# Kernel optimization log

Measured on AMD Instinct MI355X. Metric: run time of the kernel, lower is better.

Reference implementation:

```python
import jax, jax.numpy as jnp
import numpy as np

# ViT-Tiny + Performer attention (eval mode: dropout/droppath are no-ops)
B = 64
IMG, PATCH, GRID = 224, 16, 14
NPATCH, NTOK = 196, 197
EMBED, HEADS, HEAD_DIM = 192, 3, 64
DEPTH, FEAT, MLP, NCLS = 12, 256, 768, 1000
EXIT_IDXS = [4, 8, 12]
LN_EPS = 1e-5


def _ln(x, w, b):
    mu = x.mean(-1, keepdims=True)
    var = ((x - mu) ** 2).mean(-1, keepdims=True)
    return (x - mu) / jnp.sqrt(var + LN_EPS) * w + b


def setup_inputs() -> dict:
    key = jax.random.key(0)
    ks = jax.random.split(key, 16)
    n = lambda k, shape, s=0.02: jax.random.normal(k, shape, jnp.float32) * s
    inp = {}
    inp["x"] = jax.random.normal(ks[0], (B, 3, IMG, IMG), jnp.float32)
    inp["patch_w"] = n(ks[1], (EMBED, 3, PATCH, PATCH))
    inp["patch_b"] = jnp.zeros((EMBED,), jnp.float32)
    inp["pe_norm_w"] = jnp.ones((EMBED,), jnp.float32)
    inp["pe_norm_b"] = jnp.zeros((EMBED,), jnp.float32)
    inp["cls_token"] = n(ks[2], (1, 1, EMBED))
    inp["pos_embed"] = n(ks[3], (1, NTOK, EMBED))
    inp["norm1_w"] = jnp.ones((DEPTH, EMBED), jnp.float32)
    inp["norm1_b"] = jnp.zeros((DEPTH, EMBED), jnp.float32)
    inp["qkv_w"] = n(ks[4], (DEPTH, EMBED, 3 * EMBED))
    inp["qkv_b"] = jnp.zeros((DEPTH, 3 * EMBED), jnp.float32)
    # Gaussian random projection matrix (stands in for the orthogonal RF matrix)
    inp["proj_mat"] = jax.random.normal(ks[5], (DEPTH, FEAT, HEAD_DIM), jnp.float32)
    inp["attn_proj_w"] = n(ks[6], (DEPTH, EMBED, EMBED))
    inp["attn_proj_b"] = jnp.zeros((DEPTH, EMBED), jnp.float32)
    inp["norm2_w"] = jnp.ones((DEPTH, EMBED), jnp.float32)
    inp["norm2_b"] = jnp.zeros((DEPTH, EMBED), jnp.float32)
    inp["fc1_w"] = n(ks[7], (DEPTH, EMBED, MLP))
    inp["fc1_b"] = jnp.zeros((DEPTH, MLP), jnp.float32)
    inp["fc2_w"] = n(ks[8], (DEPTH, MLP, EMBED))
    inp["fc2_b"] = jnp.zeros((DEPTH, EMBED), jnp.float32)
    inp["exit_w"] = n(ks[9], (len(EXIT_IDXS), EMBED, NCLS))
    inp["exit_b"] = jnp.zeros((len(EXIT_IDXS), NCLS), jnp.float32)
    inp["final_norm_w"] = jnp.ones((EMBED,), jnp.float32)
    inp["final_norm_b"] = jnp.zeros((EMBED,), jnp.float32)
    inp["head_w"] = n(ks[10], (EMBED, NCLS))
    inp["head_b"] = jnp.zeros((NCLS,), jnp.float32)
    return inp


def _performer_attn(x, qw, qb, pm, pw, pb):
    Bn, N, C = x.shape
    qkv = (x @ qw + qb).reshape(Bn, N, 3, HEADS, HEAD_DIM).transpose(2, 0, 3, 1, 4)
    q, k, v = qkv[0], qkv[1], qkv[2]  # [B,H,N,d]

    def fmap(t):
        proj = jnp.einsum('bhnd,fd->bhnf', t, pm)  # random-feature projection
        norm_t = jnp.sum(t * t, axis=-1, keepdims=True) / 2.0
        return jnp.exp(proj - norm_t) * (HEAD_DIM ** -0.25)

    pq = fmap(q)  # [B,H,N,F]
    pk = fmap(k)
    k_cumsum = pk.sum(axis=2)  # [B,H,F]
    D_inv = 1.0 / jnp.einsum('bhnf,bhf->bhn', pq, k_cumsum)
    attn = jnp.einsum('bhnf,bhmf->bhnm', pq, pk)  # as in original (materializes NxN)
    out = jnp.einsum('bhnm,bhmd->bhnd', attn, v)
    out = out * D_inv[..., None]
    out = out.transpose(0, 2, 1, 3).reshape(Bn, N, C)
    return out @ pw + pb


def reference(x, patch_w, patch_b, pe_norm_w, pe_norm_b, cls_token, pos_embed,
              norm1_w, norm1_b, qkv_w, qkv_b, proj_mat, attn_proj_w, attn_proj_b,
              norm2_w, norm2_b, fc1_w, fc1_b, fc2_w, fc2_b,
              exit_w, exit_b, final_norm_w, final_norm_b, head_w, head_b):
    Bn = x.shape[0]
    # PatchEmbed: non-overlapping 16x16 conv == reshape + matmul (c,ph,pw order)
    p = x.reshape(Bn, 3, GRID, PATCH, GRID, PATCH).transpose(0, 2, 4, 1, 3, 5)
    p = p.reshape(Bn, NPATCH, 3 * PATCH * PATCH)
    tok = p @ patch_w.reshape(EMBED, -1).T + patch_b
    tok = _ln(tok, pe_norm_w, pe_norm_b)
    cls = jnp.broadcast_to(cls_token, (Bn, 1, EMBED))
    h = jnp.concatenate([cls, tok], axis=1) + pos_embed  # [B,197,192]

    exits = []
    for i in range(DEPTH):
        a = _performer_attn(_ln(h, norm1_w[i], norm1_b[i]), qkv_w[i], qkv_b[i],
                            proj_mat[i], attn_proj_w[i], attn_proj_b[i])
        h = h + a
        m = _ln(h, norm2_w[i], norm2_b[i])
        m = jax.nn.gelu(m @ fc1_w[i] + fc1_b[i], approximate=False) @ fc2_w[i] + fc2_b[i]
        h = h + m
        if (i + 1) in EXIT_IDXS:
            e = EXIT_IDXS.index(i + 1)
            z = h.mean(axis=1)  # AdaptiveAvgPool1d(1) over tokens
            exits.append(z @ exit_w[e] + exit_b[e])

    hf = _ln(h, final_norm_w, final_norm_b)
    logits = hf[:, 0] @ head_w + head_b  # cls-token head
    return (logits, exits[0], exits[1], exits[2])
```

## Files before the change

### kernel.cpp

```cpp
#include <hip/hip_runtime.h>
#include <math.h>

typedef unsigned short u16;
typedef unsigned int u32;
typedef __attribute__((ext_vector_type(8))) short short8;
typedef __attribute__((ext_vector_type(4))) float floatx4;

#define BB 64
#define NTOK 197
#define NPATCH 196
#define EMB 192
#define NH 3
#define HD 64
#define FEAT 256
#define MLPD 768
#define NCLS 1000
#define MTOT (BB*NTOK)
#define MPAT (BB*NPATCH)
#define BHT (BB*NH)

__device__ __forceinline__ u16 f2bf(float x) {
    u32 u = __builtin_bit_cast(u32, x);
    u32 r = u + 0x7FFFu + ((u >> 16) & 1u);
    return (u16)(r >> 16);
}
__device__ __forceinline__ float bf2f(u16 u) {
    return __builtin_bit_cast(float, (u32)u << 16);
}
__device__ __forceinline__ float sqr8bf(uint4 v) {
    float s = 0.f;
    float t;
    t = bf2f((u16)(v.x & 0xffff)); s += t*t;  t = bf2f((u16)(v.x >> 16)); s += t*t;
    t = bf2f((u16)(v.y & 0xffff)); s += t*t;  t = bf2f((u16)(v.y >> 16)); s += t*t;
    t = bf2f((u16)(v.z & 0xffff)); s += t*t;  t = bf2f((u16)(v.z >> 16)); s += t*t;
    t = bf2f((u16)(v.w & 0xffff)); s += t*t;  t = bf2f((u16)(v.w >> 16)); s += t*t;
    return s;
}

__global__ void cvt_bf16(const float* __restrict__ in, u16* __restrict__ out, int n)
{
    const int i = blockIdx.x * 256 + threadIdx.x;
    if (i < n) out[i] = f2bf(in[i]);
}

__global__ void tr_bf16_t(const float* __restrict__ in, u16* __restrict__ out,
                          int R, int C)
{
    __shared__ u16 t[32][33];
    const int l = blockIdx.z;
    const int c0 = blockIdx.x * 32, r0 = blockIdx.y * 32;
    const int tx = threadIdx.x & 31, ty = threadIdx.x >> 5;
    const float* ip = in + ((size_t)l * R + r0) * C + c0;
#pragma unroll
    for (int j = 0; j < 4; ++j)
        t[ty + j*8][tx] = f2bf(ip[(size_t)(ty + j*8) * C + tx]);
    __syncthreads();
    u16* op = out + ((size_t)l * C + c0) * R + r0;
#pragma unroll
    for (int j = 0; j < 4; ++j)
        op[(size_t)(ty + j*8) * R + tx] = t[tx][ty + j*8];
}

__global__ __launch_bounds__(256) void gemm_bf16(
    const u16* __restrict__ A, const u16* __restrict__ Bt,
    const float* __restrict__ bias,
    float* __restrict__ Cf, u16* __restrict__ Cb,
    int M, int N, int K, int mode, int ntx)
{
    __shared__ u16 As[128][72];
    __shared__ u16 Bs[64][72];
    const int tid = threadIdx.x;
    const int lane = tid & 63, wave = tid >> 6;
    const int l16 = lane & 15, quad = lane >> 4;
    const int nwg = gridDim.x;
    const int q = nwg >> 3, r = nwg & 7;
    const int xcd = blockIdx.x & 7, jj = blockIdx.x >> 3;
    const int wg = (xcd < r ? xcd * (q + 1) : r * (q + 1) + (xcd - r) * q) + jj;
// ... 73 lines not shown
        for (int cf = 0; cf < 4; ++cf) {
            const int lc = cf * 16 + l16;
            const float bia = bias[n0 + lc];
#pragma unroll
            for (int reg = 0; reg < 4; ++reg) {
                const int lr = wave * 32 + rf * 16 + quad * 4 + reg;
                float v = acc[rf][cf][reg] + bia;
                if (mode == 2)
                    v = 0.5f * v * (1.f + erff(v * 0.70710678118654752f));
                const int phys = (((lc >> 3) ^ (lr & 7)) << 3) | (lc & 7);
                As[lr][phys] = f2bf(v);
            }
        }
    }
    __syncthreads();
#pragma unroll
    for (int it = 0; it < 4; ++it) {
        const int idx = it * 256 + tid;
        const int row = idx >> 3, c8 = idx & 7;
        const int pc8 = c8 ^ (row & 7);
        const uint4 val = *(const uint4*)&As[row][pc8 * 8];
        const int gm = m0 + row;
        if (gm < M)
            *(uint4*)&Cb[(size_t)gm * N + n0 + c8 * 8] = val;
    }
}

__global__ __launch_bounds__(256) void gemm_ln(
    const u16* __restrict__ A, const u16* __restrict__ Bt,
    const float* __restrict__ bias,
    const float* __restrict__ lnw, const float* __restrict__ lnb,
    float* __restrict__ H, u16* __restrict__ outb, int K)
{
    __shared__ u16 As[64][72];
    __shared__ u16 Bs[192][72];
    __shared__ float red_s[2][64][2];
    const int tid = threadIdx.x;
    const int lane = tid & 63, wave = tid >> 6;
    const int wr = wave & 1, wc = wave >> 1;
    const int l16 = lane & 15, quad = lane >> 4;
    const int m0 = blockIdx.x * 64;
    const int srow = tid >> 2, skof = (tid & 3) * 16;

    floatx4 acc[2][6];
#pragma unroll
    for (int i = 0; i < 2; ++i)
#pragma unroll
        for (int j = 0; j < 6; ++j) acc[i][j] = (floatx4){0.f,0.f,0.f,0.f};

    const u16* ap = A + (size_t)(m0 + srow) * K + skof;
    const u16* bp = Bt + (size_t)srow * K + skof;
    const size_t bstep = (size_t)64 * K;

    for (int k0 = 0; k0 < K; k0 += 64) {
        const uint4 a0 = *(const uint4*)(ap + k0);
        const uint4 a1 = *(const uint4*)(ap + k0 + 8);
        const uint4 b0 = *(const uint4*)(bp + k0);
        const uint4 b1 = *(const uint4*)(bp + k0 + 8);
        const uint4 b2 = *(const uint4*)(bp + bstep + k0);
        const uint4 b3 = *(const uint4*)(bp + bstep + k0 + 8);
        const uint4 b4 = *(const uint4*)(bp + 2*bstep + k0);
        const uint4 b5 = *(const uint4*)(bp + 2*bstep + k0 + 8);
        if (k0) __syncthreads();
        *(uint4*)&As[srow][skof]           = a0;
        *(uint4*)&As[srow][skof + 8]       = a1;
        *(uint4*)&Bs[srow][skof]           = b0;
        *(uint4*)&Bs[srow][skof + 8]       = b1;
        *(uint4*)&Bs[srow + 64][skof]      = b2;
        *(uint4*)&Bs[srow + 64][skof + 8]  = b3;
        *(uint4*)&Bs[srow + 128][skof]     = b4;
        *(uint4*)&Bs[srow + 128][skof + 8] = b5;
        __syncthreads();
#pragma unroll
        for (int ks = 0; ks < 2; ++ks) {
            short8 af[2], bf[6];
#pragma unroll
            for (int rf = 0; rf < 2; ++rf)
                af[rf] = *(const short8*)&As[wr*32 + rf*16 + l16][ks*32 + quad*8];
#pragma unroll
            for (int cf = 0; cf < 6; ++cf)
                bf[cf] = *(const short8*)&Bs[wc*96 + cf*16 + l16][ks*32 + quad*8];
#pragma unroll
            for (int rf = 0; rf < 2; ++rf)
#pragma unroll
                for (int cf = 0; cf < 6; ++cf)
                    acc[rf][cf] = __builtin_amdgcn_mfma_f32_16x16x32_bf16(af[rf], bf[cf], acc[rf][cf], 0, 0, 0);
        }
    }

    float s_[2][4], q_[2][4];
#pragma unroll
    for (int rf = 0; rf < 2; ++rf)
#pragma unroll
        for (int reg = 0; reg < 4; ++reg) { s_[rf][reg] = 0.f; q_[rf][reg] = 0.f; }

#pragma unroll
    for (int rf = 0; rf < 2; ++rf) {
#pragma unroll
        for (int cf = 0; cf < 6; ++cf) {
            const int gn = wc * 96 + cf * 16 + l16;
            const float bia = bias[gn];
#pragma unroll
            for (int reg = 0; reg < 4; ++reg) {
                const int gm = m0 + wr * 32 + rf * 16 + quad * 4 + reg;
                float v = acc[rf][cf][reg] + bia + H[(size_t)gm * EMB + gn];
                H[(size_t)gm * EMB + gn] = v;
                acc[rf][cf][reg] = v;
                s_[rf][reg] += v;
                q_[rf][reg] += v * v;
            }
        }
    }

    if (lnw) {
#pragma unroll
        for (int rf = 0; rf < 2; ++rf)
#pragma unroll
            for (int reg = 0; reg < 4; ++reg) {
                float s = s_[rf][reg], q = q_[rf][reg];
                s += __shfl_xor(s, 1); q += __shfl_xor(q, 1);
                s += __shfl_xor(s, 2); q += __shfl_xor(q, 2);
                s += __shfl_xor(s, 4); q += __shfl_xor(q, 4);
                s += __shfl_xor(s, 8); q += __shfl_xor(q, 8);
                if (l16 == 0) {
                    const int rl = wr * 32 + rf * 16 + quad * 4 + reg;
                    red_s[wc][rl][0] = s;
                    red_s[wc][rl][1] = q;
                }
            }
        __syncthreads();
#pragma unroll
        for (int rf = 0; rf < 2; ++rf) {
#pragma unroll
            for (int reg = 0; reg < 4; ++reg) {
                const int rl = wr * 32 + rf * 16 + quad * 4 + reg;
                const float ts = red_s[0][rl][0] + red_s[1][rl][0];
                const float tq = red_s[0][rl][1] + red_s[1][rl][1];
                const float mu = ts * (1.f / 192.f);
                const float var = tq * (1.f / 192.f) - mu * mu;
                const float rstd = rsqrtf(fmaxf(var, 0.f) + 1e-5f);
                const int gm = m0 + rl;
#pragma unroll
                for (int cf = 0; cf < 6; ++cf) {
                    const int gn = wc * 96 + cf * 16 + l16;
                    const float y = (acc[rf][cf][reg] - mu) * rstd * lnw[gn] + lnb[gn];
                    outb[(size_t)gm * EMB + gn] = f2bf(y);
                }
            }
        }
    }
}

__global__ __launch_bounds__(256) void attn_pkv(
    const u16* __restrict__ qkv, const u16* __restrict__ pmb,
    u16* __restrict__ kvT, float* __restrict__ ksum)
{
    __shared__ u16 pm_s[256][72];
    __shared__ u16 kt_s[64][72];
    __shared__ u16 vT_s[64][72];
    __shared__ u16 pkT_s[256][72];
    __shared__ float nrm_s[64];
    __shared__ float ksum_s[256];

    const int tid = threadIdx.x;
    const int lane = tid & 63, wave = tid >> 6;
    const int l16 = lane & 15, quad = lane >> 4;
    const int bh = blockIdx.x, b = bh / NH, h = bh % NH;
    const int fbase = wave * 64;
    const int srow = tid >> 2, skof = (tid & 3) * 16;
    const float scale = 0.35355339059327373f;

#pragma unroll
    for (int j = 0; j < 8; ++j) {
        const int flat = j * 256 + tid;
        const int f = flat >> 3, o = (flat & 7) * 8;
        *(uint4*)&pm_s[f][o] = *(const uint4*)(pmb + f * 64 + o);
    }
    ksum_s[tid] = 0.f;

    floatx4 kv[4][4];
#pragma unroll
    for (int i = 0; i < 4; ++i)
#pragma unroll
        for (int j = 0; j < 4; ++j) kv[i][j] = (floatx4){0.f,0.f,0.f,0.f};

    uint4 k0v = {0,0,0,0}, k1v = {0,0,0,0}, v0v = {0,0,0,0}, v1v = {0,0,0,0};
    {
        const u16* kp = qkv + ((size_t)(b * NTOK + srow)) * 576 + 192 + h * 64 + skof;
        k0v = *(const uint4*)kp; k1v = *(const uint4*)(kp + 8);
        v0v = *(const uint4*)(kp + 192); v1v = *(const uint4*)(kp + 200);
    }

    for (int t = 0; t < 4; ++t) {
        const int ncur = t * 64 + srow;
        if (t) __syncthreads();
        *(uint4*)&kt_s[srow][skof]     = k0v;
        *(uint4*)&kt_s[srow][skof + 8] = k1v;
        {
            u16 vv[16];
            vv[0]=(u16)(v0v.x&0xffff);  vv[1]=(u16)(v0v.x>>16);
            vv[2]=(u16)(v0v.y&0xffff);  vv[3]=(u16)(v0v.y>>16);
            vv[4]=(u16)(v0v.z&0xffff);  vv[5]=(u16)(v0v.z>>16);
            vv[6]=(u16)(v0v.w&0xffff);  vv[7]=(u16)(v0v.w>>16);
            vv[8]=(u16)(v1v.x&0xffff);  vv[9]=(u16)(v1v.x>>16);
            vv[10]=(u16)(v1v.y&0xffff); vv[11]=(u16)(v1v.y>>16);
            vv[12]=(u16)(v1v.z&0xffff); vv[13]=(u16)(v1v.z>>16);
            vv[14]=(u16)(v1v.w&0xffff); vv[15]=(u16)(v1v.w>>16);
#pragma unroll
            for (int j = 0; j < 16; ++j) vT_s[skof + j][srow] = vv[j];
        }
        float sq = sqr8bf(k0v) + sqr8bf(k1v);
        sq += __shfl_xor(sq, 1);
        sq += __shfl_xor(sq, 2);
        if ((tid & 3) == 0) nrm_s[srow] = (ncur < NTOK) ? 0.5f * sq : 1e30f;
        __syncthreads();

        if (t < 3) {
            const int n = (t + 1) * 64 + srow;
            k0v = (uint4){0,0,0,0}; k1v = (uint4){0,0,0,0};
            v0v = (uint4){0,0,0,0}; v1v = (uint4){0,0,0,0};
            if (n < NTOK) {
                const u16* kp = qkv + ((size_t)(b * NTOK + n)) * 576 + 192 + h * 64 + skof;
                k0v = *(const uint4*)kp; k1v = *(const uint4*)(kp + 8);
                v0v = *(const uint4*)(kp + 192); v1v = *(const uint4*)(kp + 200);
            }
        }

        floatx4 pa[4][4];
#pragma unroll
        for (int i = 0; i < 4; ++i)
#pragma unroll
            for (int j = 0; j < 4; ++j) pa[i][j] = (floatx4){0.f,0.f,0.f,0.f};
#pragma unroll
        for (int ks = 0; ks < 2; ++ks) {
            short8 a[4], bb[4];
#pragma unroll
            for (int rf = 0; rf < 4; ++rf)
                a[rf] = *(const short8*)&kt_s[rf*16 + l16][ks*32 + quad*8];
#pragma unroll
            for (int cf = 0; cf < 4; ++cf)
                bb[cf] = *(const short8*)&pm_s[fbase + cf*16 + l16][ks*32 + quad*8];
#pragma unroll
            for (int rf = 0; rf < 4; ++rf)
#pragma unroll
                for (int cf = 0; cf < 4; ++cf)
                    pa[rf][cf] = __builtin_amdgcn_mfma_f32_16x16x32_bf16(a[rf], bb[cf], pa[rf][cf], 0, 0, 0);
        }

        float ksp[4] = {0.f, 0.f, 0.f, 0.f};
#pragma unroll
        for (int rf = 0; rf < 4; ++rf) {
            const int nl = rf * 16 + quad * 4;
            const float nr0 = nrm_s[nl + 0], nr1 = nrm_s[nl + 1];
            const float nr2 = nrm_s[nl + 2], nr3 = nrm_s[nl + 3];
#pragma unroll
            for (int cf = 0; cf < 4; ++cf) {
                const int f = fbase + cf * 16 + l16;
                const u16 b0 = f2bf(__expf(pa[rf][cf][0] - nr0) * scale);
                const u16 b1 = f2bf(__expf(pa[rf][cf][1] - nr1) * scale);
                const u16 b2 = f2bf(__expf(pa[rf][cf][2] - nr2) * scale);
                const u16 b3 = f2bf(__expf(pa[rf][cf][3] - nr3) * scale);
                ksp[cf] += bf2f(b0) + bf2f(b1) + bf2f(b2) + bf2f(b3);
                *(u32*)&pkT_s[f][nl]     = (u32)b0 | ((u32)b1 << 16);
                *(u32*)&pkT_s[f][nl + 2] = (u32)b2 | ((u32)b3 << 16);
            }
        }
#pragma unroll
        for (int cf = 0; cf < 4; ++cf) {
            float v = ksp[cf];
            v += __shfl_xor(v, 16);
            v += __shfl_xor(v, 32);
            if (quad == 0) ksum_s[fbase + cf*16 + l16] += v;
        }

#pragma unroll
        for (int ks = 0; ks < 2; ++ks) {
            short8 a[4], bb[4];
#pragma unroll
            for (int rf = 0; rf < 4; ++rf)
                a[rf] = *(const short8*)&vT_s[rf*16 + l16][ks*32 + quad*8];
#pragma unroll
            for (int cf = 0; cf < 4; ++cf)
                bb[cf] = *(const short8*)&pkT_s[fbase + cf*16 + l16][ks*32 + quad*8];
#pragma unroll
            for (int rf = 0; rf < 4; ++rf)
#pragma unroll
                for (int cf = 0; cf < 4; ++cf)
                    kv[rf][cf] = __builtin_amdgcn_mfma_f32_16x16x32_bf16(a[rf], bb[cf], kv[rf][cf], 0, 0, 0);
        }
    }

    __syncthreads();
    ksum[(size_t)bh * 256 + tid] = ksum_s[tid];
#pragma unroll
    for (int rf = 0; rf < 4; ++rf)
#pragma unroll
        for (int cf = 0; cf < 4; ++cf) {
            const int f = fbase + cf * 16 + l16;
#pragma unroll
            for (int reg = 0; reg < 4; ++reg) {
                const int d = rf * 16 + quad * 4 + reg;
                kvT[((size_t)bh * 64 + d) * 256 + f] = f2bf(kv[rf][cf][reg]);
            }
        }
}

__global__ __launch_bounds__(256) void attn_out(
    const u16* __restrict__ qkv, const u16* __restrict__ pmb,
    const u16* __restrict__ kvT, const float* __restrict__ ksum,
    u16* __restrict__ attn_o)
{
    __shared__ u16 pm_s[256][72];
    __shared__ u16 q_s[64][72];
    __shared__ u16 pq_s[64][264];
    __shared__ u16 kv_s[64][264];
    __shared__ float nrm_s[64];
    __shared__ float den_s[4][64];

    const int tid = threadIdx.x;
    const int lane = tid & 63, wave = tid >> 6;
    const int l16 = lane & 15, quad = lane >> 4;
    const int bh = blockIdx.y, b = bh / NH, h = bh % NH;
    const int n0 = blockIdx.x * 64;
    const int fbase = wave * 64;
    const int srow = tid >> 2, skof = (tid & 3) * 16;
    const float scale = 0.35355339059327373f;

#pragma unroll
    for (int j = 0; j < 8; ++j) {
        const int flat = j * 256 + tid;
        const int f = flat >> 3, o = (flat & 7) * 8;
        *(uint4*)&pm_s[f][o] = *(const uint4*)(pmb + f * 64 + o);
    }
#pragma unroll
    for (int j = 0; j < 8; ++j) {
        const int flat = j * 256 + tid;
        const int d = flat >> 5, o = (flat & 31) * 8;
// ... 103 lines not shown
                oc[rf][cf] = __builtin_amdgcn_mfma_f32_16x16x32_bf16(a[rf], bb[cf], oc[rf][cf], 0, 0, 0);
    }

#pragma unroll
    for (int rf = 0; rf < 2; ++rf) {
#pragma unroll
        for (int reg = 0; reg < 4; ++reg) {
            const int nl = wr*32 + rf*16 + quad*4 + reg;
            const int gn = n0 + nl;
            if (gn >= NTOK) continue;
            const float di = 1.f / (den_s[0][nl] + den_s[1][nl] + den_s[2][nl] + den_s[3][nl]);
#pragma unroll
            for (int cf = 0; cf < 2; ++cf) {
                const int d = wc*32 + cf*16 + l16;
                attn_o[((size_t)(b * NTOK + gn)) * EMB + h * 64 + d] =
                    f2bf(oc[rf][cf][reg] * di);
            }
        }
    }
}

__global__ void im2col_kernel(const float* __restrict__ x, u16* __restrict__ p, int total)
{
    const int i = blockIdx.x * 256 + threadIdx.x;
    if (i >= total) return;
    const int col = i % 768, row = i / 768;
    const int px = col & 15, py = (col >> 4) & 15, c = col >> 8;
    const int gx = row % 14, gy = (row / 14) % 14, b = row / 196;
    p[i] = f2bf(x[((size_t)(b * 3 + c) * 224 + gy * 16 + py) * 224 + gx * 16 + px]);
}

__global__ void embed_finish(const float* __restrict__ tok, const float* __restrict__ cls,
                             const float* __restrict__ pos, const float* __restrict__ w,
                             const float* __restrict__ b, float* __restrict__ h)
{
    const int wid = threadIdx.x >> 6, lane = threadIdx.x & 63;
    const int r = blockIdx.x * 4 + wid;
    if (r >= MTOT) return;
    const int bb = r / NTOK, t = r % NTOK;
    float* q = h + (size_t)r * EMB;
    if (t == 0) {
        q[lane]       = cls[lane]       + pos[lane];
        q[lane + 64]  = cls[lane + 64]  + pos[lane + 64];
        q[lane + 128] = cls[lane + 128] + pos[lane + 128];
        return;
    }
    const float* p = tok + ((size_t)bb * NPATCH + (t - 1)) * EMB;
    float x0 = p[lane], x1 = p[lane + 64], x2 = p[lane + 128];
    float s = x0 + x1 + x2;
#pragma unroll
    for (int off = 32; off; off >>= 1) s += __shfl_xor(s, off);
    const float mu = s * (1.f / 192.f);
    const float d0 = x0 - mu, d1 = x1 - mu, d2 = x2 - mu;
    float v = d0 * d0 + d1 * d1 + d2 * d2;
#pragma unroll
    for (int off = 32; off; off >>= 1) v += __shfl_xor(v, off);
    const float rstd = rsqrtf(v * (1.f / 192.f) + 1e-5f);
    const float* pr = pos + (size_t)t * EMB;
    q[lane]       = d0 * rstd * w[lane]       + b[lane]       + pr[lane];
    q[lane + 64]  = d1 * rstd * w[lane + 64]  + b[lane + 64]  + pr[lane + 64];
    q[lane + 128] = d2 * rstd * w[lane + 128] + b[lane + 128] + pr[lane + 128];
}

__global__ void ln192(const float* __restrict__ in, int in_stride,
                      const float* __restrict__ w, const float* __restrict__ b,
                      u16* __restrict__ outb, float* __restrict__ outf, int rows)
{
    const int wid = threadIdx.x >> 6, lane = threadIdx.x & 63;
    const int r = blockIdx.x * 4 + wid;
    if (r >= rows) return;
    const float* p = in + (size_t)r * in_stride;
    float x0 = p[lane], x1 = p[lane + 64], x2 = p[lane + 128];
    float s = x0 + x1 + x2;
#pragma unroll
    for (int off = 32; off; off >>= 1) s += __shfl_xor(s, off);
    const float mu = s * (1.f / 192.f);
    const float d0 = x0 - mu, d1 = x1 - mu, d2 = x2 - mu;
    float v = d0 * d0 + d1 * d1 + d2 * d2;
#pragma unroll
    for (int off = 32; off; off >>= 1) v += __shfl_xor(v, off);
    const float rstd = rsqrtf(v * (1.f / 192.f) + 1e-5f);
    const float y0 = d0 * rstd * w[lane]       + b[lane];
    const float y1 = d1 * rstd * w[lane + 64]  + b[lane + 64];
    const float y2 = d2 * rstd * w[lane + 128] + b[lane + 128];
    if (outf) {
        float* q = outf + (size_t)r * EMB;
        q[lane] = y0; q[lane + 64] = y1; q[lane + 128] = y2;
    } else {
        u16* q = outb + (size_t)r * EMB;
        q[lane] = f2bf(y0); q[lane + 64] = f2bf(y1); q[lane + 128] = f2bf(y2);
    }
}

__global__ __launch_bounds__(256) void gemm_f32(
    const float* __restrict__ A, const float* __restrict__ Bm,
    const float* __restrict__ bias, float* __restrict__ C,
    int M, int N, int K)
{
    __shared__ float As[16][68];
    __shared__ float Bs[16][64];
    const int tid = threadIdx.x;
    const int tx = tid & 15, ty = tid >> 4;
    const int m0 = blockIdx.y * 64, n0 = blockIdx.x * 64;
    float acc[4][4] = {};

    for (int k0 = 0; k0 < K; k0 += 16) {
        {
            const int c = tid & 15, r4 = tid >> 4;
#pragma unroll
            for (int i = 0; i < 4; ++i) {
                const int r = r4 + i * 16, gm = m0 + r;
                As[c][r] = (gm < M) ? A[(size_t)gm * K + (k0 + c)] : 0.f;
            }
        }
        {
            const int cb = tid & 63, rb4 = tid >> 6;
#pragma unroll
            for (int i = 0; i < 4; ++i) {
                const int rb = rb4 + i * 4;
                const int gn = n0 + cb;
                Bs[rb][cb] = (gn < N) ? Bm[(size_t)(k0 + rb) * N + gn] : 0.f;
            }
        }
        __syncthreads();
#pragma unroll
        for (int kk = 0; kk < 16; ++kk) {
            const float4 av = *reinterpret_cast<const float4*>(&As[kk][ty * 4]);
            const float4 bv = *reinterpret_cast<const float4*>(&Bs[kk][tx * 4]);
            const float a_[4] = {av.x, av.y, av.z, av.w};
            const float b_[4] = {bv.x, bv.y, bv.z, bv.w};
#pragma unroll
            for (int i2 = 0; i2 < 4; ++i2)
#pragma unroll
                for (int j2 = 0; j2 < 4; ++j2)
                    acc[i2][j2] = fmaf(a_[i2], b_[j2], acc[i2][j2]);
        }
        __syncthreads();
    }

#pragma unroll
    for (int i = 0; i < 4; ++i) {
        const int gm = m0 + ty * 4 + i;
        if (gm >= M) continue;
#pragma unroll
        for (int j = 0; j < 4; ++j) {
            const int gn = n0 + tx * 4 + j;
            if (gn >= N) continue;
            C[(size_t)gm * N + gn] = acc[i][j] + bias[gn];
        }
    }
}

__global__ void pool_kernel(const float* __restrict__ h, float* __restrict__ pooled)
{
    __shared__ float red[192];
    const int b = blockIdx.x;
    const int slice = threadIdx.x / 192;
    const int e = threadIdx.x % 192;
    float s = 0.f;
    for (int n = slice; n < NTOK; n += 2)
        s += h[((size_t)(b * NTOK + n)) * EMB + e];
    if (slice == 1) red[e] = s;
    __syncthreads();
    if (slice == 0)
        pooled[b * EMB + e] = (s + red[e]) * (1.f / 197.f);
}

extern "C" void kernel_launch(void* const* d_in, const int* in_sizes, int n_in,
                              void* d_out, int out_size, void* d_ws, size_t ws_size,
                              hipStream_t stream)
{
    const float* x          = (const float*)d_in[0];
    const float* patch_w    = (const float*)d_in[1];
    const float* patch_b    = (const float*)d_in[2];
    const float* pe_norm_w  = (const float*)d_in[3];
    const float* pe_norm_b  = (const float*)d_in[4];
    const float* cls_token  = (const float*)d_in[5];
    const float* pos_embed  = (const float*)d_in[6];
    const float* norm1_w    = (const float*)d_in[7];
    const float* norm1_b    = (const float*)d_in[8];
    const float* qkv_w      = (const float*)d_in[9];
    const float* qkv_b      = (const float*)d_in[10];
    const float* proj_mat   = (const float*)d_in[11];
    const float* attn_pw    = (const float*)d_in[12];
    const float* attn_pb    = (const float*)d_in[13];
    const float* norm2_w    = (const float*)d_in[14];
    const float* norm2_b    = (const float*)d_in[15];
    const float* fc1_w      = (const float*)d_in[16];
    const float* fc1_b      = (const float*)d_in[17];
    const float* fc2_w      = (const float*)d_in[18];
    const float* fc2_b      = (const float*)d_in[19];
    const float* exit_w     = (const float*)d_in[20];
    const float* exit_b     = (const float*)d_in[21];
    const float* fnorm_w    = (const float*)d_in[22];
    const float* fnorm_b    = (const float*)d_in[23];
    const float* head_w     = (const float*)d_in[24];
    const float* head_b     = (const float*)d_in[25];
    float* out = (float*)d_out;

    float* ws = (float*)d_ws;
    float* H     = ws + 0;
    u16*   QKVB  = (u16*)(ws + 2420736);
    u16*   XLNB  = (u16*)(ws + 6051840);
    u16*   KVT   = (u16*)(ws + 19968000);
    u16*   MIDB  = (u16*)(ws + 21540864);
    u16*   ATNB  = (u16*)(ws + 26382336);
    float* XLNF  = ws + 27592704;
    float* POOL  = ws + 27604992;
    float* KSUM  = ws + 27617280;
    u16*   QKVWT = (u16*)(ws + 27666432);
    u16*   APWT  = (u16*)(ws + 28329984);
    u16*   F1WT  = (u16*)(ws + 28551168);
    u16*   F2WT  = (u16*)(ws + 29435904);
    u16*   PATWB = (u16*)(ws + 30320640);
    u16*   PMB   = (u16*)(ws + 30394368);
    u16*   P_IMB = MIDB;
    float* TOK   = (float*)QKVB;

    if (ws_size < (size_t)30492672 * sizeof(float)) return;

    cvt_bf16<<<(147456 + 255) / 256, 256, 0, stream>>>(patch_w, PATWB, 147456);
    cvt_bf16<<<(196608 + 255) / 256, 256, 0, stream>>>(proj_mat, PMB, 196608);
    tr_bf16_t<<<dim3(18, 6, 12), 256, 0, stream>>>(qkv_w,   QKVWT, 192, 576);
    tr_bf16_t<<<dim3(6, 6, 12),  256, 0, stream>>>(attn_pw, APWT,  192, 192);
    tr_bf16_t<<<dim3(24, 6, 12), 256, 0, stream>>>(fc1_w,   F1WT,  192, 768);
    tr_bf16_t<<<dim3(6, 24, 12), 256, 0, stream>>>(fc2_w,   F2WT,  768, 192);

    im2col_kernel<<<(MPAT * 768 + 255) / 256, 256, 0, stream>>>(x, P_IMB, MPAT * 768);
    gemm_bf16<<<294, 256, 0, stream>>>(P_IMB, PATWB, patch_b,
                                       TOK, nullptr, MPAT, EMB, 768, 0, 3);
    embed_finish<<<(MTOT + 3) / 4, 256, 0, stream>>>(TOK, cls_token, pos_embed,
                                                     pe_norm_w, pe_norm_b, H);
    ln192<<<(MTOT + 3) / 4, 256, 0, stream>>>(H, EMB, norm1_w, norm1_b,
                                              XLNB, nullptr, MTOT);

    for (int i = 0; i < 12; ++i) {
        const u16* qwt  = QKVWT + (size_t)i * 576 * 192;
        const u16* pwt  = APWT  + (size_t)i * 192 * 192;
        const u16* f1wt = F1WT  + (size_t)i * 768 * 192;
        const u16* f2wt = F2WT  + (size_t)i * 192 * 768;
        const u16* pmb  = PMB   + (size_t)i * 256 * 64;
        const float* qb  = qkv_b   + (size_t)i * 576;
        const float* pb  = attn_pb + (size_t)i * 192;
        const float* f1b = fc1_b   + (size_t)i * 768;
        const float* f2b = fc2_b   + (size_t)i * 192;

        gemm_bf16<<<891, 256, 0, stream>>>(XLNB, qwt, qb,
                                           nullptr, QKVB, MTOT, 576, 192, 3, 9);
        attn_pkv<<<dim3(BHT), 256, 0, stream>>>(QKVB, pmb, KVT, KSUM);
        attn_out<<<dim3(4, BHT), 256, 0, stream>>>(QKVB, pmb, KVT, KSUM, ATNB);
        gemm_ln<<<197, 256, 0, stream>>>(ATNB, pwt, pb,
                                         norm2_w + (size_t)i * EMB, norm2_b + (size_t)i * EMB,
                                         H, XLNB, EMB);
        gemm_bf16<<<1188, 256, 0, stream>>>(XLNB, f1wt, f1b,
                                            nullptr, MIDB, MTOT, MLPD, 192, 2, 12);
        const float* nw = (i < 11) ? norm1_w + (size_t)(i + 1) * EMB : nullptr;
        const float* nb = (i < 11) ? norm1_b + (size_t)(i + 1) * EMB : nullptr;
        gemm_ln<<<197, 256, 0, stream>>>(MIDB, f2wt, f2b, nw, nb, H, XLNB, MLPD);

        const int e = (i == 3) ? 0 : (i == 7) ? 1 : (i == 11) ? 2 : -1;
        if (e >= 0) {
            pool_kernel<<<BB, 384, 0, stream>>>(H, POOL);
            gemm_f32<<<dim3(16, 1), 256, 0, stream>>>(POOL, exit_w + (size_t)e * 192 * 1000,
                                                      exit_b + (size_t)e * 1000,
                                                      out + (size_t)(1 + e) * BB * NCLS,
                                                      BB, NCLS, EMB);
        }
    }

    ln192<<<(BB + 3) / 4, 256, 0, stream>>>(H, NTOK * EMB, fnorm_w, fnorm_b,
                                            nullptr, XLNF, BB);
    gemm_f32<<<dim3(16, 1), 256, 0, stream>>>(XLNF, head_w, head_b, out, BB, NCLS, EMB);
}
```

Before: 1.540 ms.

## Split attention and LN-GEMM across more blocks, fuse embed LN, MFMA classifier heads

Several changes land together. gemm_ln tiles are cut from 64 to 32 rows, doubling the grid to 394 blocks, and attn_pkv is split across four feature-quarter blocks per batch-head, both to raise occupancy on a GPU with many CUs. The first norm1 LayerNorm is folded into embed_finish, which removes one launch and one pass over H. The fp32 exit and head GEMMs become bf16 MFMA kernels on pre-transposed weights, at some cost in precision for the classifier outputs.

Measured after the change: 1.391 ms. 1.11x faster.

```diff
diff --git a/kernel.cpp b/kernel.cpp
--- a/kernel.cpp
+++ b/kernel.cpp
@@ -43,6 +43,17 @@
     if (i < n) out[i] = f2bf(in[i]);
 }
 
+__global__ void tr_bf16(const float* __restrict__ in, u16* __restrict__ out,
+                        int R, int C, int total)
+{
+    const int i = blockIdx.x * 256 + threadIdx.x;
+    if (i >= total) return;
+    const int r = i % R;
+    const int c = (i / R) % C;
+    const int l = i / (R * C);
+    out[i] = f2bf(in[((size_t)l * R + r) * C + c]);
+}
+
 __global__ void tr_bf16_t(const float* __restrict__ in, u16* __restrict__ out,
                           int R, int C)
 {
@@ -182,29 +193,28 @@
     const float* __restrict__ lnw, const float* __restrict__ lnb,
     float* __restrict__ H, u16* __restrict__ outb, int K)
 {
-    __shared__ u16 As[64][72];
+    __shared__ u16 As[32][72];
     __shared__ u16 Bs[192][72];
-    __shared__ float red_s[2][64][2];
+    __shared__ float red_s[2][32][2];
     const int tid = threadIdx.x;
     const int lane = tid & 63, wave = tid >> 6;
-    const int wr = wave & 1, wc = wave >> 1;
+    const int wr = wave & 1;
+    const int wc = wave >> 1;
     const int l16 = lane & 15, quad = lane >> 4;
-    const int m0 = blockIdx.x * 64;
+    const int m0 = blockIdx.x * 32;
+    const int srowA = tid >> 3, skofA = (tid & 7) * 8;
     const int srow = tid >> 2, skof = (tid & 3) * 16;
 
-    floatx4 acc[2][6];
-#pragma unroll
-    for (int i = 0; i < 2; ++i)
-#pragma unroll
-        for (int j = 0; j < 6; ++j) acc[i][j] = (floatx4){0.f,0.f,0.f,0.f};
-
-    const u16* ap = A + (size_t)(m0 + srow) * K + skof;
+    floatx4 acc[6];
+#pragma unroll
+    for (int j = 0; j < 6; ++j) acc[j] = (floatx4){0.f,0.f,0.f,0.f};
+
+    const u16* ap = A + (size_t)(m0 + srowA) * K + skofA;
     const u16* bp = Bt + (size_t)srow * K + skof;
     const size_t bstep = (size_t)64 * K;
 
     for (int k0 = 0; k0 < K; k0 += 64) {
         const uint4 a0 = *(const uint4*)(ap + k0);
-        const uint4 a1 = *(const uint4*)(ap + k0 + 8);
         const uint4 b0 = *(const uint4*)(bp + k0);
         const uint4 b1 = *(const uint4*)(bp + k0 + 8);
         const uint4 b2 = *(const uint4*)(bp + bstep + k0);
@@ -212,8 +222,7 @@
         const uint4 b4 = *(const uint4*)(bp + 2*bstep + k0);
         const uint4 b5 = *(const uint4*)(bp + 2*bstep + k0 + 8);
         if (k0) __syncthreads();
-        *(uint4*)&As[srow][skof]           = a0;
-        *(uint4*)&As[srow][skof + 8]       = a1;
+        *(uint4*)&As[srowA][skofA]         = a0;
         *(uint4*)&Bs[srow][skof]           = b0;
         *(uint4*)&Bs[srow][skof + 8]       = b1;
         *(uint4*)&Bs[srow + 64][skof]      = b2;
@@ -223,79 +232,65 @@
         __syncthreads();
 #pragma unroll
         for (int ks = 0; ks < 2; ++ks) {
-            short8 af[2], bf[6];
-#pragma unroll
-            for (int rf = 0; rf < 2; ++rf)
-                af[rf] = *(const short8*)&As[wr*32 + rf*16 + l16][ks*32 + quad*8];
+            const short8 af = *(const short8*)&As[wr*16 + l16][ks*32 + quad*8];
+            short8 bf[6];
 #pragma unroll
             for (int cf = 0; cf < 6; ++cf)
                 bf[cf] = *(const short8*)&Bs[wc*96 + cf*16 + l16][ks*32 + quad*8];
 #pragma unroll
-            for (int rf = 0; rf < 2; ++rf)
-#pragma unroll
-                for (int cf = 0; cf < 6; ++cf)
-                    acc[rf][cf] = __builtin_amdgcn_mfma_f32_16x16x32_bf16(af[rf], bf[cf], acc[rf][cf], 0, 0, 0);
-        }
-    }
-
-    float s_[2][4], q_[2][4];
-#pragma unroll
-    for (int rf = 0; rf < 2; ++rf)
-#pragma unroll
-        for (int reg = 0; reg < 4; ++reg) { s_[rf][reg] = 0.f; q_[rf][reg] = 0.f; }
-
-#pragma unroll
-    for (int rf = 0; rf < 2; ++rf) {
-#pragma unroll
-        for (int cf = 0; cf < 6; ++cf) {
-            const int gn = wc * 96 + cf * 16 + l16;
-            const float bia = bias[gn];
-#pragma unroll
-            for (int reg = 0; reg < 4; ++reg) {
-                const int gm = m0 + wr * 32 + rf * 16 + quad * 4 + reg;
-                float v = acc[rf][cf][reg] + bia + H[(size_t)gm * EMB + gn];
-                H[(size_t)gm * EMB + gn] = v;
-                acc[rf][cf][reg] = v;
-                s_[rf][reg] += v;
-                q_[rf][reg] += v * v;
+            for (int cf = 0; cf < 6; ++cf)
+                acc[cf] = __builtin_amdgcn_mfma_f32_16x16x32_bf16(af, bf[cf], acc[cf], 0, 0, 0);
+        }
+    }
+
+    float s_[4], q_[4];
+#pragma unroll
+    for (int reg = 0; reg < 4; ++reg) { s_[reg] = 0.f; q_[reg] = 0.f; }
+
+#pragma unroll
+    for (int cf = 0; cf < 6; ++cf) {
+        const int gn = wc * 96 + cf * 16 + l16;
+        const float bia = bias[gn];
+#pragma unroll
+        for (int reg = 0; reg < 4; ++reg) {
+            const int gm = m0 + wr * 16 + quad * 4 + reg;
+            float v = acc[cf][reg] + bia + H[(size_t)gm * EMB + gn];
+            H[(size_t)gm * EMB + gn] = v;
+            acc[cf][reg] = v;
+            s_[reg] += v;
+            q_[reg] += v * v;
+        }
+    }
+
+    if (lnw) {
+#pragma unroll
+        for (int reg = 0; reg < 4; ++reg) {
+            float s = s_[reg], q = q_[reg];
+            s += __shfl_xor(s, 1); q += __shfl_xor(q, 1);
+            s += __shfl_xor(s, 2); q += __shfl_xor(q, 2);
+            s += __shfl_xor(s, 4); q += __shfl_xor(q, 4);
+            s += __shfl_xor(s, 8); q += __shfl_xor(q, 8);
+            if (l16 == 0) {
+                const int rl = wr * 16 + quad * 4 + reg;
+                red_s[wc][rl][0] = s;
+                red_s[wc][rl][1] = q;
             }
         }
-    }
-
-    if (lnw) {
-#pragma unroll
-        for (int rf = 0; rf < 2; ++rf)
-#pragma unroll
-            for (int reg = 0; reg < 4; ++reg) {
-                float s = s_[rf][reg], q = q_[rf][reg];
-                s += __shfl_xor(s, 1); q += __shfl_xor(q, 1);
-                s += __shfl_xor(s, 2); q += __shfl_xor(q, 2);
-                s += __shfl_xor(s, 4); q += __shfl_xor(q, 4);
-                s += __shfl_xor(s, 8); q += __shfl_xor(q, 8);
-                if (l16 == 0) {
-                    const int rl = wr * 32 + rf * 16 + quad * 4 + reg;
-                    red_s[wc][rl][0] = s;
-                    red_s[wc][rl][1] = q;
-                }
-            }
         __syncthreads();
 #pragma unroll
-        for (int rf = 0; rf < 2; ++rf) {
-#pragma unroll
-            for (int reg = 0; reg < 4; ++reg) {
-                const int rl = wr * 32 + rf * 16 + quad * 4 + reg;
-                const float ts = red_s[0][rl][0] + red_s[1][rl][0];
-                const float tq = red_s[0][rl][1] + red_s[1][rl][1];
-                const float mu = ts * (1.f / 192.f);
-                const float var = tq * (1.f / 192.f) - mu * mu;
-                const float rstd = rsqrtf(fmaxf(var, 0.f) + 1e-5f);
-                const int gm = m0 + rl;
-#pragma unroll
-                for (int cf = 0; cf < 6; ++cf) {
-                    const int gn = wc * 96 + cf * 16 + l16;
-                    const float y = (acc[rf][cf][reg] - mu) * rstd * lnw[gn] + lnb[gn];
-                    outb[(size_t)gm * EMB + gn] = f2bf(y);
-                }
+        for (int reg = 0; reg < 4; ++reg) {
+            const int rl = wr * 16 + quad * 4 + reg;
+            const float ts = red_s[0][rl][0] + red_s[1][rl][0];
+            const float tq = red_s[0][rl][1] + red_s[1][rl][1];
+            const float mu = ts * (1.f / 192.f);
+            const float var = tq * (1.f / 192.f) - mu * mu;
+            const float rstd = rsqrtf(fmaxf(var, 0.f) + 1e-5f);
+            const int gm = m0 + rl;
+#pragma unroll
+            for (int cf = 0; cf < 6; ++cf) {
+                const int gn = wc * 96 + cf * 16 + l16;
+                const float y = (acc[cf][reg] - mu) * rstd * lnw[gn] + lnb[gn];
+                outb[(size_t)gm * EMB + gn] = f2bf(y);
             }
         }
     }
@@ -305,34 +300,32 @@
     const u16* __restrict__ qkv, const u16* __restrict__ pmb,
     u16* __restrict__ kvT, float* __restrict__ ksum)
 {
-    __shared__ u16 pm_s[256][72];
+    __shared__ u16 pm_s[64][72];
     __shared__ u16 kt_s[64][72];
     __shared__ u16 vT_s[64][72];
-    __shared__ u16 pkT_s[256][72];
+    __shared__ u16 pkT_s[64][72];
     __shared__ float nrm_s[64];
-    __shared__ float ksum_s[256];
+    __shared__ float ksum_s[64];
 
     const int tid = threadIdx.x;
     const int lane = tid & 63, wave = tid >> 6;
     const int l16 = lane & 15, quad = lane >> 4;
-    const int bh = blockIdx.x, b = bh / NH, h = bh % NH;
-    const int fbase = wave * 64;
+    const int fq = blockIdx.x, bh = blockIdx.y, b = bh / NH, h = bh % NH;
+    const int fwave = wave * 16;
     const int srow = tid >> 2, skof = (tid & 3) * 16;
     const float scale = 0.35355339059327373f;
 
 #pragma unroll
-    for (int j = 0; j < 8; ++j) {
+    for (int j = 0; j < 2; ++j) {
         const int flat = j * 256 + tid;
-        const int f = flat >> 3, o = (flat & 7) * 8;
-        *(uint4*)&pm_s[f][o] = *(const uint4*)(pmb + f * 64 + o);
-    }
-    ksum_s[tid] = 0.f;
-
-    floatx4 kv[4][4];
-#pragma unroll
-    for (int i = 0; i < 4; ++i)
-#pragma unroll
-        for (int j = 0; j < 4; ++j) kv[i][j] = (floatx4){0.f,0.f,0.f,0.f};
+        const int row = flat >> 3, o = (flat & 7) * 8;
+        *(uint4*)&pm_s[row][o] = *(const uint4*)(pmb + (size_t)(fq * 64 + row) * 64 + o);
+    }
+    if (tid < 64) ksum_s[tid] = 0.f;
+
+    floatx4 kv[4];
+#pragma unroll
+    for (int i = 0; i < 4; ++i) kv[i] = (floatx4){0.f,0.f,0.f,0.f};
 
     uint4 k0v = {0,0,0,0}, k1v = {0,0,0,0}, v0v = {0,0,0,0}, v1v = {0,0,0,0};
     {
@@ -376,83 +369,61 @@
             }
         }
 
-        floatx4 pa[4][4];
-#pragma unroll
-        for (int i = 0; i < 4; ++i)
-#pragma unroll
-            for (int j = 0; j < 4; ++j) pa[i][j] = (floatx4){0.f,0.f,0.f,0.f};
+        floatx4 pa[4];
+#pragma unroll
+        for (int i = 0; i < 4; ++i) pa[i] = (floatx4){0.f,0.f,0.f,0.f};
 #pragma unroll
         for (int ks = 0; ks < 2; ++ks) {
-            short8 a[4], bb[4];
-#pragma unroll
-            for (int rf = 0; rf < 4; ++rf)
-                a[rf] = *(const short8*)&kt_s[rf*16 + l16][ks*32 + quad*8];
-#pragma unroll
-            for (int cf = 0; cf < 4; ++cf)
-                bb[cf] = *(const short8*)&pm_s[fbase + cf*16 + l16][ks*32 + quad*8];
-#pragma unroll
-            for (int rf = 0; rf < 4; ++rf)
-#pragma unroll
-                for (int cf = 0; cf < 4; ++cf)
-                    pa[rf][cf] = __builtin_amdgcn_mfma_f32_16x16x32_bf16(a[rf], bb[cf], pa[rf][cf], 0, 0, 0);
-        }
-
-        float ksp[4] = {0.f, 0.f, 0.f, 0.f};
+            const short8 bpm = *(const short8*)&pm_s[fwave + l16][ks*32 + quad*8];
+#pragma unroll
+            for (int rf = 0; rf < 4; ++rf) {
+                const short8 a = *(const short8*)&kt_s[rf*16 + l16][ks*32 + quad*8];
+                pa[rf] = __builtin_amdgcn_mfma_f32_16x16x32_bf16(a, bpm, pa[rf], 0, 0, 0);
+            }
+        }
+
+        float ksp = 0.f;
+        const int floc = fwave + l16;
 #pragma unroll
         for (int rf = 0; rf < 4; ++rf) {
             const int nl = rf * 16 + quad * 4;
-            const float nr0 = nrm_s[nl + 0], nr1 = nrm_s[nl + 1];
-            const float nr2 = nrm_s[nl + 2], nr3 = nrm_s[nl + 3];
-#pragma unroll
-            for (int cf = 0; cf < 4; ++cf) {
-                const int f = fbase + cf * 16 + l16;
-                const u16 b0 = f2bf(__expf(pa[rf][cf][0] - nr0) * scale);
-                const u16 b1 = f2bf(__expf(pa[rf][cf][1] - nr1) * scale);
-                const u16 b2 = f2bf(__expf(pa[rf][cf][2] - nr2) * scale);
-                const u16 b3 = f2bf(__expf(pa[rf][cf][3] - nr3) * scale);
-                ksp[cf] += bf2f(b0) + bf2f(b1) + bf2f(b2) + bf2f(b3);
-                *(u32*)&pkT_s[f][nl]     = (u32)b0 | ((u32)b1 << 16);
-                *(u32*)&pkT_s[f][nl + 2] = (u32)b2 | ((u32)b3 << 16);
-            }
-        }
-#pragma unroll
-        for (int cf = 0; cf < 4; ++cf) {
-            float v = ksp[cf];
+            const u16 b0 = f2bf(__expf(pa[rf][0] - nrm_s[nl + 0]) * scale);
+            const u16 b1 = f2bf(__expf(pa[rf][1] - nrm_s[nl + 1]) * scale);
+            const u16 b2 = f2bf(__expf(pa[rf][2] - nrm_s[nl + 2]) * scale);
+            const u16 b3 = f2bf(__expf(pa[rf][3] - nrm_s[nl + 3]) * scale);
+            ksp += bf2f(b0) + bf2f(b1) + bf2f(b2) + bf2f(b3);
+            *(u32*)&pkT_s[floc][nl]     = (u32)b0 | ((u32)b1 << 16);
+            *(u32*)&pkT_s[floc][nl + 2] = (u32)b2 | ((u32)b3 << 16);
+        }
+        {
+            float v = ksp;
             v += __shfl_xor(v, 16);
             v += __shfl_xor(v, 32);
-            if (quad == 0) ksum_s[fbase + cf*16 + l16] += v;
+            if (quad == 0) ksum_s[floc] += v;
         }
 
 #pragma unroll
         for (int ks = 0; ks < 2; ++ks) {
-            short8 a[4], bb[4];
-#pragma unroll
-            for (int rf = 0; rf < 4; ++rf)
-                a[rf] = *(const short8*)&vT_s[rf*16 + l16][ks*32 + quad*8];
-#pragma unroll
-            for (int cf = 0; cf < 4; ++cf)
-                bb[cf] = *(const short8*)&pkT_s[fbase + cf*16 + l16][ks*32 + quad*8];
-#pragma unroll
-            for (int rf = 0; rf < 4; ++rf)
-#pragma unroll
-                for (int cf = 0; cf < 4; ++cf)
-                    kv[rf][cf] = __builtin_amdgcn_mfma_f32_16x16x32_bf16(a[rf], bb[cf], kv[rf][cf], 0, 0, 0);
+            const short8 bpk = *(const short8*)&pkT_s[fwave + l16][ks*32 + quad*8];
+#pragma unroll
+            for (int rf = 0; rf < 4; ++rf) {
+                const short8 a = *(const short8*)&vT_s[rf*16 + l16][ks*32 + quad*8];
+                kv[rf] = __builtin_amdgcn_mfma_f32_16x16x32_bf16(a, bpk, kv[rf], 0, 0, 0);
+            }
         }
     }
 
     __syncthreads();
-    ksum[(size_t)bh * 256 + tid] = ksum_s[tid];
-#pragma unroll
-    for (int rf = 0; rf < 4; ++rf)
-#pragma unroll
-        for (int cf = 0; cf < 4; ++cf) {
-            const int f = fbase + cf * 16 + l16;
-#pragma unroll
-            for (int reg = 0; reg < 4; ++reg) {
-                const int d = rf * 16 + quad * 4 + reg;
-                kvT[((size_t)bh * 64 + d) * 256 + f] = f2bf(kv[rf][cf][reg]);
-            }
-        }
+    if (tid < 64) ksum[(size_t)bh * 256 + fq * 64 + tid] = ksum_s[tid];
+    const int fg = fq * 64 + fwave + l16;
+#pragma unroll
+    for (int rf = 0; rf < 4; ++rf) {
+#pragma unroll
+        for (int reg = 0; reg < 4; ++reg) {
+            const int d = rf * 16 + quad * 4 + reg;
+            kvT[((size_t)bh * 64 + d) * 256 + fg] = f2bf(kv[rf][reg]);
+        }
+    }
 }
 
 __global__ __launch_bounds__(256) void attn_out(
@@ -622,34 +593,51 @@
 
 __global__ void embed_finish(const float* __restrict__ tok, const float* __restrict__ cls,
                              const float* __restrict__ pos, const float* __restrict__ w,
-                             const float* __restrict__ b, float* __restrict__ h)
+                             const float* __restrict__ b,
+                             const float* __restrict__ n1w, const float* __restrict__ n1b,
+                             float* __restrict__ h, u16* __restrict__ outb)
 {
     const int wid = threadIdx.x >> 6, lane = threadIdx.x & 63;
     const int r = blockIdx.x * 4 + wid;
     if (r >= MTOT) return;
     const int bb = r / NTOK, t = r % NTOK;
+    float y0, y1, y2;
+    if (t == 0) {
+        y0 = cls[lane]       + pos[lane];
+        y1 = cls[lane + 64]  + pos[lane + 64];
+        y2 = cls[lane + 128] + pos[lane + 128];
+    } else {
+        const float* p = tok + ((size_t)bb * NPATCH + (t - 1)) * EMB;
+        float x0 = p[lane], x1 = p[lane + 64], x2 = p[lane + 128];
+        float s = x0 + x1 + x2;
+#pragma unroll
+        for (int off = 32; off; off >>= 1) s += __shfl_xor(s, off);
+        const float mu = s * (1.f / 192.f);
+        const float d0 = x0 - mu, d1 = x1 - mu, d2 = x2 - mu;
+        float v = d0 * d0 + d1 * d1 + d2 * d2;
+#pragma unroll
+        for (int off = 32; off; off >>= 1) v += __shfl_xor(v, off);
+        const float rstd = rsqrtf(v * (1.f / 192.f) + 1e-5f);
+        const float* pr = pos + (size_t)t * EMB;
+        y0 = d0 * rstd * w[lane]       + b[lane]       + pr[lane];
+        y1 = d1 * rstd * w[lane + 64]  + b[lane + 64]  + pr[lane + 64];
+        y2 = d2 * rstd * w[lane + 128] + b[lane + 128] + pr[lane + 128];
+    }
     float* q = h + (size_t)r * EMB;
-    if (t == 0) {
-        q[lane]       = cls[lane]       + pos[lane];
-        q[lane + 64]  = cls[lane + 64]  + pos[lane + 64];
-        q[lane + 128] = cls[lane + 128] + pos[lane + 128];
-        return;
-    }
-    const float* p = tok + ((size_t)bb * NPATCH + (t - 1)) * EMB;
-    float x0 = p[lane], x1 = p[lane + 64], x2 = p[lane + 128];
-    float s = x0 + x1 + x2;
-#pragma unroll
-    for (int off = 32; off; off >>= 1) s += __shfl_xor(s, off);
-    const float mu = s * (1.f / 192.f);
-    const float d0 = x0 - mu, d1 = x1 - mu, d2 = x2 - mu;
-    float v = d0 * d0 + d1 * d1 + d2 * d2;
-#pragma unroll
-    for (int off = 32; off; off >>= 1) v += __shfl_xor(v, off);
-    const float rstd = rsqrtf(v * (1.f / 192.f) + 1e-5f);
-    const float* pr = pos + (size_t)t * EMB;
-    q[lane]       = d0 * rstd * w[lane]       + b[lane]       + pr[lane];
-    q[lane + 64]  = d1 * rstd * w[lane + 64]  + b[lane + 64]  + pr[lane + 64];
-    q[lane + 128] = d2 * rstd * w[lane + 128] + b[lane + 128] + pr[lane + 128];
+    q[lane] = y0; q[lane + 64] = y1; q[lane + 128] = y2;
+    float s2 = y0 + y1 + y2;
+#pragma unroll
+    for (int off = 32; off; off >>= 1) s2 += __shfl_xor(s2, off);
+    const float mu2 = s2 * (1.f / 192.f);
+    const float e0 = y0 - mu2, e1 = y1 - mu2, e2 = y2 - mu2;
+    float v2 = e0 * e0 + e1 * e1 + e2 * e2;
+#pragma unroll
+    for (int off = 32; off; off >>= 1) v2 += __shfl_xor(v2, off);
+    const float rstd2 = rsqrtf(v2 * (1.f / 192.f) + 1e-5f);
+    u16* o = outb + (size_t)r * EMB;
+    o[lane]       = f2bf(e0 * rstd2 * n1w[lane]       + n1b[lane]);
+    o[lane + 64]  = f2bf(e1 * rstd2 * n1w[lane + 64]  + n1b[lane + 64]);
+    o[lane + 128] = f2bf(e2 * rstd2 * n1w[lane + 128] + n1b[lane + 128]);
 }
 
 __global__ void ln192(const float* __restrict__ in, int in_stride,
@@ -682,66 +670,74 @@
     }
 }
 
-__global__ __launch_bounds__(256) void gemm_f32(
-    const float* __restrict__ A, const float* __restrict__ Bm,
+__global__ __launch_bounds__(256) void gemm_cls(
+    const u16* __restrict__ A, const u16* __restrict__ Bt,
     const float* __restrict__ bias, float* __restrict__ C,
-    int M, int N, int K)
-{
-    __shared__ float As[16][68];
-    __shared__ float Bs[16][64];
+    int N, int K)
+{
+    __shared__ u16 As[64][72];
+    __shared__ u16 Bs[64][72];
     const int tid = threadIdx.x;
-    const int tx = tid & 15, ty = tid >> 4;
-    const int m0 = blockIdx.y * 64, n0 = blockIdx.x * 64;
-    float acc[4][4] = {};
-
-    for (int k0 = 0; k0 < K; k0 += 16) {
-        {
-            const int c = tid & 15, r4 = tid >> 4;
-#pragma unroll
-            for (int i = 0; i < 4; ++i) {
-                const int r = r4 + i * 16, gm = m0 + r;
-                As[c][r] = (gm < M) ? A[(size_t)gm * K + (k0 + c)] : 0.f;
+    const int lane = tid & 63, wave = tid >> 6;
+    const int wr = wave & 1, wc = wave >> 1;
+    const int l16 = lane & 15, quad = lane >> 4;
+    const int n0 = blockIdx.x * 64;
+    const int srow = tid >> 2, skof = (tid & 3) * 16;
+
+    floatx4 acc[2][2];
+#pragma unroll
+    for (int i = 0; i < 2; ++i)
+#pragma unroll
+        for (int j = 0; j < 2; ++j) acc[i][j] = (floatx4){0.f,0.f,0.f,0.f};
+
+    const u16* ap = A + (size_t)srow * K + skof;
+    int brow_g = n0 + srow;  if (brow_g > N - 1) brow_g = N - 1;
+    const u16* bp = Bt + (size_t)brow_g * K + skof;
+
+    for (int k0 = 0; k0 < K; k0 += 64) {
+        const uint4 a0 = *(const uint4*)(ap + k0);
+        const uint4 a1 = *(const uint4*)(ap + k0 + 8);
+        const uint4 b0 = *(const uint4*)(bp + k0);
+        const uint4 b1 = *(const uint4*)(bp + k0 + 8);
+        if (k0) __syncthreads();
+        *(uint4*)&As[srow][skof]     = a0;
+        *(uint4*)&As[srow][skof + 8] = a1;
+        *(uint4*)&Bs[srow][skof]     = b0;
+        *(uint4*)&Bs[srow][skof + 8] = b1;
+        __syncthreads();
+#pragma unroll
+        for (int ks = 0; ks < 2; ++ks) {
+            short8 af[2], bf[2];
+#pragma unroll
+            for (int rf = 0; rf < 2; ++rf)
+                af[rf] = *(const short8*)&As[wr*32 + rf*16 + l16][ks*32 + quad*8];
+#pragma unroll
+            for (int cf = 0; cf < 2; ++cf)
+                bf[cf] = *(const short8*)&Bs[wc*32 + cf*16 + l16][ks*32 + quad*8];
+#pragma unroll
+            for (int rf = 0; rf < 2; ++rf)
+#pragma unroll
+                for (int cf = 0; cf < 2; ++cf)
+                    acc[rf][cf] = __builtin_amdgcn_mfma_f32_16x16x32_bf16(af[rf], bf[cf], acc[rf][cf], 0, 0, 0);
+        }
+    }
+
+#pragma unroll
+    for (int rf = 0; rf < 2; ++rf) {
+#pragma unroll
+        for (int reg = 0; reg < 4; ++reg) {
+            const int gm = wr*32 + rf*16 + quad*4 + reg;
+#pragma unroll
+            for (int cf = 0; cf < 2; ++cf) {
+                const int gn = n0 + wc*32 + cf*16 + l16;
+                if (gn < N)
+                    C[(size_t)gm * N + gn] = acc[rf][cf][reg] + bias[gn];
             }
         }
-        {
-            const int cb = tid & 63, rb4 = tid >> 6;
-#pragma unroll
-            for (int i = 0; i < 4; ++i) {
-                const int rb = rb4 + i * 4;
-                const int gn = n0 + cb;
-                Bs[rb][cb] = (gn < N) ? Bm[(size_t)(k0 + rb) * N + gn] : 0.f;
-            }
-        }
-        __syncthreads();
-#pragma unroll
-        for (int kk = 0; kk < 16; ++kk) {
-            const float4 av = *reinterpret_cast<const float4*>(&As[kk][ty * 4]);
-            const float4 bv = *reinterpret_cast<const float4*>(&Bs[kk][tx * 4]);
-            const float a_[4] = {av.x, av.y, av.z, av.w};
-            const float b_[4] = {bv.x, bv.y, bv.z, bv.w};
-#pragma unroll
-            for (int i2 = 0; i2 < 4; ++i2)
-#pragma unroll
-                for (int j2 = 0; j2 < 4; ++j2)
-                    acc[i2][j2] = fmaf(a_[i2], b_[j2], acc[i2][j2]);
-        }
-        __syncthreads();
-    }
-
-#pragma unroll
-    for (int i = 0; i < 4; ++i) {
-        const int gm = m0 + ty * 4 + i;
-        if (gm >= M) continue;
-#pragma unroll
-        for (int j = 0; j < 4; ++j) {
-            const int gn = n0 + tx * 4 + j;
-            if (gn >= N) continue;
-            C[(size_t)gm * N + gn] = acc[i][j] + bias[gn];
-        }
-    }
-}
-
-__global__ void pool_kernel(const float* __restrict__ h, float* __restrict__ pooled)
+    }
+}
+
+__global__ void pool_kernel(const float* __restrict__ h, u16* __restrict__ pooled)
 {
     __shared__ float red[192];
     const int b = blockIdx.x;
@@ -753,7 +749,7 @@
     if (slice == 1) red[e] = s;
     __syncthreads();
     if (slice == 0)
-        pooled[b * EMB + e] = (s + red[e]) * (1.f / 197.f);
+        pooled[b * EMB + e] = f2bf((s + red[e]) * (1.f / 197.f));
 }
 
 extern "C" void kernel_launch(void* const* d_in, const int* in_sizes, int n_in,
@@ -792,11 +788,12 @@
     float* H     = ws + 0;
     u16*   QKVB  = (u16*)(ws + 2420736);
     u16*   XLNB  = (u16*)(ws + 6051840);
+    u16*   EXWT  = (u16*)(ws + 7262208);
+    u16*   HWT   = (u16*)(ws + 7550208);
+    u16*   POOLB = (u16*)(ws + 7646208);
     u16*   KVT   = (u16*)(ws + 19968000);
     u16*   MIDB  = (u16*)(ws + 21540864);
     u16*   ATNB  = (u16*)(ws + 26382336);
-    float* XLNF  = ws + 27592704;
-    float* POOL  = ws + 27604992;
     float* KSUM  = ws + 27617280;
     u16*   QKVWT = (u16*)(ws + 27666432);
     u16*   APWT  = (u16*)(ws + 28329984);
@@ -815,14 +812,15 @@
     tr_bf16_t<<<dim3(6, 6, 12),  256, 0, stream>>>(attn_pw, APWT,  192, 192);
     tr_bf16_t<<<dim3(24, 6, 12), 256, 0, stream>>>(fc1_w,   F1WT,  192, 768);
     tr_bf16_t<<<dim3(6, 24, 12), 256, 0, stream>>>(fc2_w,   F2WT,  768, 192);
+    tr_bf16<<<(576000 + 255) / 256, 256, 0, stream>>>(exit_w, EXWT, 192, 1000, 576000);
+    tr_bf16<<<(192000 + 255) / 256, 256, 0, stream>>>(head_w, HWT,  192, 1000, 192000);
 
     im2col_kernel<<<(MPAT * 768 + 255) / 256, 256, 0, stream>>>(x, P_IMB, MPAT * 768);
     gemm_bf16<<<294, 256, 0, stream>>>(P_IMB, PATWB, patch_b,
                                        TOK, nullptr, MPAT, EMB, 768, 0, 3);
     embed_finish<<<(MTOT + 3) / 4, 256, 0, stream>>>(TOK, cls_token, pos_embed,
-                                                     pe_norm_w, pe_norm_b, H);
-    ln192<<<(MTOT + 3) / 4, 256, 0, stream>>>(H, EMB, norm1_w, norm1_b,
-                                              XLNB, nullptr, MTOT);
+                                                     pe_norm_w, pe_norm_b,
+                                                     norm1_w, norm1_b, H, XLNB);
 
     for (int i = 0; i < 12; ++i) {
         const u16* qwt  = QKVWT + (size_t)i * 576 * 192;
@@ -833,32 +831,32 @@
         const float* qb  = qkv_b   + (size_t)i * 576;
         const float* pb  = attn_pb + (size_t)i * 192;
         const float* f1b = fc1_b   + (size_t)i * 768;
-        const float* f2b = fc2_b   + (size_t)i * 192;
 
         gemm_bf16<<<891, 256, 0, stream>>>(XLNB, qwt, qb,
                                            nullptr, QKVB, MTOT, 576, 192, 3, 9);
-        attn_pkv<<<dim3(BHT), 256, 0, stream>>>(QKVB, pmb, KVT, KSUM);
+        attn_pkv<<<dim3(4, BHT), 256, 0, stream>>>(QKVB, pmb, KVT, KSUM);
         attn_out<<<dim3(4, BHT), 256, 0, stream>>>(QKVB, pmb, KVT, KSUM, ATNB);
-        gemm_ln<<<197, 256, 0, stream>>>(ATNB, pwt, pb,
+        gemm_ln<<<394, 256, 0, stream>>>(ATNB, pwt, pb,
                                          norm2_w + (size_t)i * EMB, norm2_b + (size_t)i * EMB,
                                          H, XLNB, EMB);
         gemm_bf16<<<1188, 256, 0, stream>>>(XLNB, f1wt, f1b,
                                             nullptr, MIDB, MTOT, MLPD, 192, 2, 12);
         const float* nw = (i < 11) ? norm1_w + (size_t)(i + 1) * EMB : nullptr;
         const float* nb = (i < 11) ? norm1_b + (size_t)(i + 1) * EMB : nullptr;
-        gemm_ln<<<197, 256, 0, stream>>>(MIDB, f2wt, f2b, nw, nb, H, XLNB, MLPD);
+        gemm_ln<<<394, 256, 0, stream>>>(MIDB, f2wt, fc2_b + (size_t)i * 192,
+                                         nw, nb, H, XLNB, MLPD);
 
         const int e = (i == 3) ? 0 : (i == 7) ? 1 : (i == 11) ? 2 : -1;
         if (e >= 0) {
-            pool_kernel<<<BB, 384, 0, stream>>>(H, POOL);
-            gemm_f32<<<dim3(16, 1), 256, 0, stream>>>(POOL, exit_w + (size_t)e * 192 * 1000,
-                                                      exit_b + (size_t)e * 1000,
-                                                      out + (size_t)(1 + e) * BB * NCLS,
-                                                      BB, NCLS, EMB);
+            pool_kernel<<<BB, 384, 0, stream>>>(H, POOLB);
+            gemm_cls<<<16, 256, 0, stream>>>(POOLB, EXWT + (size_t)e * 1000 * 192,
+                                             exit_b + (size_t)e * 1000,
+                                             out + (size_t)(1 + e) * BB * NCLS,
+                                             NCLS, EMB);
         }
     }
 
     ln192<<<(BB + 3) / 4, 256, 0, stream>>>(H, NTOK * EMB, fnorm_w, fnorm_b,
-                                            nullptr, XLNF, BB);
-    gemm_f32<<<dim3(16, 1), 256, 0, stream>>>(XLNF, head_w, head_b, out, BB, NCLS, EMB);
-}
+                                            XLNB, nullptr, BB);
+    gemm_cls<<<16, 256, 0, stream>>>(XLNB, HWT, head_b, out, NCLS, EMB);
+}
```
